# Performance work log

Measured on AMD Instinct MI355X. Metric: run time of the kernel, lower is better.

The kernel has to match this reference:

```python
import jax, jax.numpy as jnp
import numpy as np

B, T, F, H = 64, 128, 1024, 1024
FORGET_BIAS = 1.0  # TF BasicLSTMCell default


def setup_inputs() -> dict:
    key = jax.random.key(0)
    k1, k2 = jax.random.split(key, 2)
    x = jax.random.normal(k1, (B, T, F), dtype=jnp.float32)
    # single fused kernel weight [(F+H), 4H], TF gate order: i, j, f, o
    W = jax.random.uniform(k2, (F + H, 4 * H), dtype=jnp.float32, minval=-0.1, maxval=0.1)
    b = jnp.zeros((4 * H,), dtype=jnp.float32)
    return {"x": x, "W": W, "b": b}


def reference(x, W, b):
    # BasicLSTMCell unrolled over time (return_last=False, return_seq_2d=False)
    batch, n_steps, n_feat = x.shape
    n_hidden = W.shape[0] - n_feat

    def step(carry, xt):
        c, h = carry
        z = jnp.concatenate([xt, h], axis=1) @ W + b  # [B, 4H]
        i, j, f, o = jnp.split(z, 4, axis=1)
        c_new = c * jax.nn.sigmoid(f + FORGET_BIAS) + jax.nn.sigmoid(i) * jnp.tanh(j)
        h_new = jnp.tanh(c_new) * jax.nn.sigmoid(o)
        return (c_new, h_new), h_new

    c0 = jnp.zeros((batch, n_hidden), x.dtype)
    h0 = jnp.zeros((batch, n_hidden), x.dtype)
    _, hs = jax.lax.scan(step, (c0, h0), jnp.swapaxes(x, 0, 1))  # [T, B, H]
    return jnp.swapaxes(hs, 0, 1)  # [B, T, H]
```

## Files before the change

### kernel.cpp

```cpp
#include <hip/hip_runtime.h>
#include <hip/hip_bf16.h>

typedef unsigned short u16;
typedef unsigned int u32;
typedef unsigned long long u64;
typedef __bf16 bf16x8 __attribute__((ext_vector_type(8)));
typedef float f32x4 __attribute__((ext_vector_type(4)));

#define NB 64
#define NT 128
#define NF 1024
#define NH 1024
#define NK 2048
#define NG 4096
#define NBH (NB * NH)

#define FSTR 16

#define W_LDS_BYTES 131072
#define ZSX_BYTES (2 * 2 * 64 * 17 * 4)
#define ZSH_BYTES (2 * 64 * 17 * 4)
#define SMEM_BYTES (W_LDS_BYTES + ZSX_BYTES + ZSH_BYTES + 64)

__device__ __forceinline__ u16 f2bf(float f) {
  unsigned u = __builtin_bit_cast(unsigned, f);
  u = (u + 0x7FFFu + ((u >> 16) & 1u)) >> 16;
  return (u16)u;
}
__device__ __forceinline__ float bf2f(u16 v) {
  unsigned u = ((unsigned)v) << 16;
  return __builtin_bit_cast(float, u);
}

__global__ __launch_bounds__(256) void lstm_cvt_x(const float* __restrict__ x,
                                                  u16* __restrict__ xb) {
  int i = (blockIdx.x * 256 + threadIdx.x) * 4;
  float4 v = *reinterpret_cast<const float4*>(x + i);
  ushort4 o;
  o.x = f2bf(v.x); o.y = f2bf(v.y); o.z = f2bf(v.z); o.w = f2bf(v.w);
  *reinterpret_cast<ushort4*>(xb + i) = o;
}

__global__ __launch_bounds__(256) void lstm_prep_w(const float* __restrict__ W,
                                                   u16* __restrict__ wt_blk) {
  __shared__ float tile[32][33];
  int n0 = blockIdx.x * 32;
  int k0 = blockIdx.y * 32;
  int tc = threadIdx.x & 31;
  int tr = threadIdx.x >> 5;
#pragma unroll
  for (int i = 0; i < 4; ++i) {
    int k = tr + i * 8;
    tile[k][tc] = W[(size_t)(k0 + k) * NG + n0 + tc];
  }
  __syncthreads();
#pragma unroll
  for (int i = 0; i < 4; ++i) {
    int n = n0 + tr + i * 8;
    float wv = tile[tc][tr + i * 8];
    int k = k0 + tc;
    int g = n >> 10, col = n & 1023;
    int b = col >> 2, brow = g * 4 + (col & 3);
    int kh = k >> 10, ch = (k & 1023) >> 5;
    int slot = (k >> 3) & 3, elem = k & 7;
    size_t base = (size_t)b * 65536 + (size_t)(kh * 32 + ch) * 512
                + (size_t)(slot * 16 + brow) * 8 + elem;
    u16 hi = f2bf(wv);
    wt_blk[base] = hi;
    wt_blk[base + 32768] = f2bf(wv - bf2f(hi));
  }
}

__device__ __forceinline__ void mfma_pass(const u16* __restrict__ a0, size_t rstride,
                                          const u16* __restrict__ Wl, int khalf,
                                          int kq, int lane, f32x4 acc[4]) {
  bf16x8 pf[4], qf[4];
#pragma unroll
  for (int i = 0; i < 4; ++i)
    pf[i] = *reinterpret_cast<const bf16x8*>(a0 + (size_t)i * 16 * rstride);
#pragma unroll
  for (int cc = 0; cc < 8; ++cc) {
    if (cc < 7) {
#pragma unroll
      for (int i = 0; i < 4; ++i)
        qf[i] = *reinterpret_cast<const bf16x8*>(a0 + (size_t)i * 16 * rstride + (cc + 1) * 32);
    }
    const int ch = kq * 8 + cc;
    const bf16x8 wh = *reinterpret_cast<const bf16x8*>(
        Wl + (size_t)(khalf * 32 + ch) * 512 + lane * 8);
    const bf16x8 wl2 = *reinterpret_cast<const bf16x8*>(
        Wl + (size_t)(64 + khalf * 32 + ch) * 512 + lane * 8);
#pragma unroll
    for (int i = 0; i < 4; ++i)
      acc[i] = __builtin_amdgcn_mfma_f32_16x16x32_bf16(pf[i], wh, acc[i], 0, 0, 0);
#pragma unroll
    for (int i = 0; i < 4; ++i)
      acc[i] = __builtin_amdgcn_mfma_f32_16x16x32_bf16(pf[i], wl2, acc[i], 0, 0, 0);
#pragma unroll
    for (int i = 0; i < 4; ++i) pf[i] = qf[i];
  }
}

__global__ __launch_bounds__(512) void lstm_persist(
    const u16* __restrict__ xb, u16* __restrict__ hseq,
    const u16* __restrict__ wt_blk, const float* __restrict__ bias,
    float* __restrict__ out, u32* __restrict__ flags,
    float* __restrict__ zo) {
  extern __shared__ char smem[];
  u16* Wl = (u16*)smem;
  float (*zsx)[2][64][17] = (float(*)[2][64][17])(smem + W_LDS_BYTES);
  float (*zsh)[64][17] = (float(*)[64][17])(smem + W_LDS_BYTES + ZSX_BYTES);
  volatile u32* hsflag = (volatile u32*)(smem + W_LDS_BYTES + ZSX_BYTES + ZSH_BYTES);

  const int b = blockIdx.x;
  const int tid = threadIdx.x;
  const int lane = tid & 63;
  const int w = tid >> 6;
  const bool is_x = (w < 4);
  const int kq = w & 3;

  {
    const u16* src = wt_blk + (size_t)b * 65536;
#pragma unroll
    for (int it = 0; it < 16; ++it) {
      uint4 v = *reinterpret_cast<const uint4*>(src + (size_t)it * 4096 + tid * 8);
      *reinterpret_cast<uint4*>(Wl + (size_t)it * 4096 + tid * 8) = v;
    }
  }
  for (int i = tid; i < 2 * 64 * 17; i += 512) ((float*)zsh)[i] = 0.f;
  if (tid == 0) hsflag[0] = 0u;

  const int arow = lane & 15;
  const int kfr = 8 * (lane >> 4);
  const int kbase = kq * 256 + kfr;
  const int zn = lane & 15;
  const int mg = (lane >> 4) * 4;

  const int prow = tid >> 1;
  const int pc = (tid & 1) * 2;
  const int gc0 = b * 4 + pc;
  float bz[2][4];
  float creg[2] = {0.f, 0.f};
  if (tid < 128) {
#pragma unroll
    for (int j = 0; j < 2; ++j) {
      bz[j][0] = bias[gc0 + j];
      bz[j][1] = bias[NH + gc0 + j];
      bz[j][2] = bias[2 * NH + gc0 + j];
      bz[j][3] = bias[3 * NH + gc0 + j];
    }
  }
  __syncthreads();

  {
    f32x4 acc[4] = {};
    if (is_x) {
      const u16* a0 = xb + ((size_t)arow * NT + 0) * NF + kbase;
      mfma_pass(a0, (size_t)NT * NF, Wl, 0, kq, lane, acc);
      if (w < 2) {
#pragma unroll
        for (int i = 0; i < 4; ++i)
#pragma unroll
          for (int r = 0; r < 4; ++r) zsx[0][w][i * 16 + mg + r][zn] = acc[i][r];
      }
    }
    __syncthreads();
    if (is_x && w >= 2) {
#pragma unroll
      for (int i = 0; i < 4; ++i)
#pragma unroll
        for (int r = 0; r < 4; ++r) zsx[0][w - 2][i * 16 + mg + r][zn] += acc[i][r];
    }
    __syncthreads();
  }

#pragma unroll 1
  for (int t = 0; t < NT; ++t) {
    const int cb = t & 1;
    const int nb = (t + 1) & 1;
    f32x4 acc[4] = {};

    if (is_x) {
      if (t < NT - 1) {
        const u16* a0 = xb + ((size_t)arow * NT + (t + 1)) * NF + kbase;
        mfma_pass(a0, (size_t)NT * NF, Wl, 0, kq, lane, acc);
      }
    } else {
      if (t > 0) {
        const u32* fp = flags + ((size_t)t * 256 + kq * 64 + lane) * FSTR;
        u32 v = __hip_atomic_load(fp, __ATOMIC_RELAXED, __HIP_MEMORY_SCOPE_AGENT);
        while (!__all(v != 0)) {
          __builtin_amdgcn_s_sleep(1);
          v = __hip_atomic_load(fp, __ATOMIC_RELAXED, __HIP_MEMORY_SCOPE_AGENT);
        }

        const u64* hb = reinterpret_cast<const u64*>(hseq) + (size_t)t * (256 * 64);
        const int sbase = kq * 64 + 2 * (lane >> 4);
        u64 plo[4], phi[4], qlo[4], qhi[4];
#pragma unroll
        for (int i = 0; i < 4; ++i) {
          plo[i] = hb[(size_t)sbase * 64 + arow + 16 * i];
          phi[i] = hb[(size_t)(sbase + 1) * 64 + arow + 16 * i];
        }
        __builtin_amdgcn_s_setprio(1);
#pragma unroll
        for (int cc = 0; cc < 8; ++cc) {
          if (cc < 7) {
            const int s = sbase + (cc + 1) * 8;
#pragma unroll
            for (int i = 0; i < 4; ++i) {
              qlo[i] = hb[(size_t)s * 64 + arow + 16 * i];
              qhi[i] = hb[(size_t)(s + 1) * 64 + arow + 16 * i];
            }
          }
          const int ch = kq * 8 + cc;
          const bf16x8 wh = *reinterpret_cast<const bf16x8*>(
              Wl + (size_t)(32 + ch) * 512 + lane * 8);
          const bf16x8 wlo = *reinterpret_cast<const bf16x8*>(
              Wl + (size_t)(96 + ch) * 512 + lane * 8);
#pragma unroll
          for (int i = 0; i < 4; ++i) {
            union HU { u64 q[2]; bf16x8 f; } u;
            u.q[0] = plo[i];
            u.q[1] = phi[i];
            acc[i] = __builtin_amdgcn_mfma_f32_16x16x32_bf16(u.f, wh, acc[i], 0, 0, 0);
            acc[i] = __builtin_amdgcn_mfma_f32_16x16x32_bf16(u.f, wlo, acc[i], 0, 0, 0);
          }
#pragma unroll
          for (int i = 0; i < 4; ++i) { plo[i] = qlo[i]; phi[i] = qhi[i]; }
        }
        __builtin_amdgcn_s_setprio(0);
      }
    }

    if (is_x) {
      if (w < 2 && t < NT - 1) {
#pragma unroll
        for (int i = 0; i < 4; ++i)
#pragma unroll
          for (int r = 0; r < 4; ++r) zsx[nb][w][i * 16 + mg + r][zn] = acc[i][r];
      }
    } else {
      if (w < 6 && t > 0) {
#pragma unroll
        for (int i = 0; i < 4; ++i)
#pragma unroll
          for (int r = 0; r < 4; ++r) zsh[w - 4][i * 16 + mg + r][zn] = acc[i][r];
      }
    }
    __syncthreads();
    if (is_x) {
      if (w >= 2 && t < NT - 1) {
#pragma unroll
        for (int i = 0; i < 4; ++i)
#pragma unroll
          for (int r = 0; r < 4; ++r) zsx[nb][w - 2][i * 16 + mg + r][zn] += acc[i][r];
      }
    } else {
      if (w >= 6 && t > 0) {
#pragma unroll
        for (int i = 0; i < 4; ++i)
#pragma unroll
          for (int r = 0; r < 4; ++r) zsh[w - 6][i * 16 + mg + r][zn] += acc[i][r];
      }
    }
    __syncthreads();

    if (tid < 128) {
      float hn[2];
#pragma unroll
      for (int jj = 0; jj < 2; ++jj) {
        const int col = pc + jj;
        const float zi = zsx[cb][0][prow][col]      + zsx[cb][1][prow][col]      + zsh[0][prow][col]      + zsh[1][prow][col]      + bz[jj][0];
        const float zj = zsx[cb][0][prow][4 + col]  + zsx[cb][1][prow][4 + col]  + zsh[0][prow][4 + col]  + zsh[1][prow][4 + col]  + bz[jj][1];
        const float zf = zsx[cb][0][prow][8 + col]  + zsx[cb][1][prow][8 + col]  + zsh[0][prow][8 + col]  + zsh[1][prow][8 + col]  + bz[jj][2];
        const float zo4 = zsx[cb][0][prow][12 + col] + zsx[cb][1][prow][12 + col] + zsh[0][prow][12 + col] + zsh[1][prow][12 + col] + bz[jj][3];
        const float si = 1.f / (1.f + __expf(-zi));
        const float tj = tanhf(zj);
        const float sf = 1.f / (1.f + __expf(-(zf + 1.0f)));
        const float so = 1.f / (1.f + __expf(-zo4));
        const float cn = creg[jj] * sf + si * tj;
        hn[jj] = tanhf(cn) * so;
        creg[jj] = cn;
      }
      if (t < NT - 1) {
        u32 hv = (u32)f2bf(hn[0]) | ((u32)f2bf(hn[1]) << 16);
        u32* hp = reinterpret_cast<u32*>(hseq)
                + ((size_t)(t + 1) * 256 + b) * 128 + prow * 2 + (pc >> 1);
        __hip_atomic_store(hp, hv, __ATOMIC_RELAXED, __HIP_MEMORY_SCOPE_AGENT);
        asm volatile("s_waitcnt vmcnt(0)" ::: "memory");
        if (tid == 64) hsflag[0] = (u32)(t + 1);
        if (tid == 0) {
          while (hsflag[0] != (u32)(t + 1)) {}
          __hip_atomic_store(&flags[((size_t)(t + 1) * 256 + b) * FSTR], 1u,
                             __ATOMIC_RELAXED, __HIP_MEMORY_SCOPE_AGENT);
        }
      }
#pragma unroll
      for (int jj = 0; jj < 2; ++jj) {
        __hip_atomic_store(
            reinterpret_cast<u32*>(zo + ((size_t)t * NH + gc0 + jj) * NB + prow),
            __builtin_bit_cast(u32, hn[jj]),
            __ATOMIC_RELAXED, __HIP_MEMORY_SCOPE_AGENT);
      }
    }
  }

  __syncthreads();
  asm volatile("s_waitcnt vmcnt(0)" ::: "memory");
  if (tid == 0)
    __hip_atomic_store(&flags[(size_t)b * FSTR], 1u, __ATOMIC_RELAXED,
                       __HIP_MEMORY_SCOPE_AGENT);
  if (w == 0) {
    bool ok;
    do {
      u32 v0 = __hip_atomic_load(flags + (size_t)(lane * 4 + 0) * FSTR, __ATOMIC_RELAXED, __HIP_MEMORY_SCOPE_AGENT);
      u32 v1 = __hip_atomic_load(flags + (size_t)(lane * 4 + 1) * FSTR, __ATOMIC_RELAXED, __HIP_MEMORY_SCOPE_AGENT);
      u32 v2 = __hip_atomic_load(flags + (size_t)(lane * 4 + 2) * FSTR, __ATOMIC_RELAXED, __HIP_MEMORY_SCOPE_AGENT);
      u32 v3 = __hip_atomic_load(flags + (size_t)(lane * 4 + 3) * FSTR, __ATOMIC_RELAXED, __HIP_MEMORY_SCOPE_AGENT);
      ok = ((v0 & v1 & v2 & v3) == 1u);
      if (!__all(ok)) __builtin_amdgcn_s_sleep(1);
    } while (!__all(ok));
  }
  __syncthreads();

  {
    const int ts = b >> 1;
    const int r0 = (b & 1) * 32;
    float* T = (float*)smem;
#pragma unroll 4
    for (int it = 0; it < 16; ++it) {
      int flat = it * 512 + tid;
      int c = flat >> 3;
      int q = flat & 7;
      const u64* p = reinterpret_cast<const u64*>(
          zo + ((size_t)ts * NH + c) * NB + r0 + q * 4);
      u64 lo = __hip_atomic_load(p + 0, __ATOMIC_RELAXED, __HIP_MEMORY_SCOPE_AGENT);
      u64 hi = __hip_atomic_load(p + 1, __ATOMIC_RELAXED, __HIP_MEMORY_SCOPE_AGENT);
      T[(q * 4 + 0) * 1028 + c] = __builtin_bit_cast(float, (u32)lo);
      T[(q * 4 + 1) * 1028 + c] = __builtin_bit_cast(float, (u32)(lo >> 32));
      T[(q * 4 + 2) * 1028 + c] = __builtin_bit_cast(float, (u32)hi);
      T[(q * 4 + 3) * 1028 + c] = __builtin_bit_cast(float, (u32)(hi >> 32));
    }
    __syncthreads();
#pragma unroll 4
    for (int it = 0; it < 16; ++it) {
      int flat = it * 512 + tid;
      int r = flat >> 8;
      int c4 = flat & 255;
      float4 v;
      v.x = T[r * 1028 + c4 * 4 + 0];
      v.y = T[r * 1028 + c4 * 4 + 1];
      v.z = T[r * 1028 + c4 * 4 + 2];
      v.w = T[r * 1028 + c4 * 4 + 3];
      *reinterpret_cast<float4*>(
          out + ((size_t)(r0 + r) * NT + ts) * NH + c4 * 4) = v;
    }
  }
}

extern "C" void kernel_launch(void* const* d_in, const int* in_sizes, int n_in,
                              void* d_out, int out_size, void* d_ws, size_t ws_size,
                              hipStream_t stream) {
  const float* x = (const float*)d_in[0];
  const float* W = (const float*)d_in[1];
  const float* bias = (const float*)d_in[2];
  float* out = (float*)d_out;

  char* ws = (char*)d_ws;
  u16* xb = (u16*)(ws);
  u16* wt_blk = (u16*)(ws + 16777216);
  u16* hseq = (u16*)(ws + 50331648);
  u32* flags = (u32*)(ws + 67108864);
  float* zo = (float*)(ws + 69206016);

  hipMemsetAsync(hseq, 0, 256 * 512, stream);
  hipMemsetAsync(flags, 0, (size_t)NT * 256 * FSTR * 4, stream);

  lstm_cvt_x<<<(NB * NT * NF) / (256 * 4), 256, 0, stream>>>(x, xb);
  lstm_prep_w<<<dim3(NG / 32, NK / 32), 256, 0, stream>>>(W, wt_blk);

  hipFuncSetAttribute((const void*)lstm_persist,
                      hipFuncAttributeMaxDynamicSharedMemorySize, SMEM_BYTES);

  void* args[] = {(void*)&xb, (void*)&hseq, (void*)&wt_blk, (void*)&bias,
                  (void*)&out, (void*)&flags, (void*)&zo};
  hipLaunchCooperativeKernel((void*)lstm_persist, dim3(256), dim3(512), args,
                             SMEM_BYTES, stream);
}
```

Before: 1.038 ms.

## Reduce gate partials with LDS atomics and drop a per-step barrier

Replaces the two-stage store-then-add reduction of x and h gate partials into separate LDS buffers with float atomicAdd into a single double-buffered accumulator. One __syncthreads per timestep is removed. The x-waves now wait on per-wave release flags written by the pointwise waves after they zero the buffer slot, so the next step's x projection can overlap the pointwise phase. The cost is LDS atomic contention from eight waves adding into the same cells, and a reduction order that is no longer fixed.

```diff
diff --git a/kernel.cpp b/kernel.cpp
--- a/kernel.cpp
+++ b/kernel.cpp
@@ -18,9 +18,18 @@
 #define FSTR 16
 
 #define W_LDS_BYTES 131072
-#define ZSX_BYTES (2 * 2 * 64 * 17 * 4)
-#define ZSH_BYTES (2 * 64 * 17 * 4)
-#define SMEM_BYTES (W_LDS_BYTES + ZSX_BYTES + ZSH_BYTES + 64)
+#define ZS_BYTES (2 * 64 * 17 * 4)
+#define SMEM_BYTES (W_LDS_BYTES + ZS_BYTES + 64)
+
+__device__ __forceinline__ void st_rel(u32* p, u32 v) {
+  __hip_atomic_store(p, v, __ATOMIC_RELEASE, __HIP_MEMORY_SCOPE_WORKGROUP);
+}
+__device__ __forceinline__ u32 ld_acq(u32* p) {
+  return __hip_atomic_load(p, __ATOMIC_ACQUIRE, __HIP_MEMORY_SCOPE_WORKGROUP);
+}
+__device__ __forceinline__ void spin_ge(u32* p, u32 v) {
+  while (ld_acq(p) < v) {}
+}
 
 __device__ __forceinline__ u16 f2bf(float f) {
   unsigned u = __builtin_bit_cast(unsigned, f);
@@ -108,9 +117,8 @@
     float* __restrict__ zo) {
   extern __shared__ char smem[];
   u16* Wl = (u16*)smem;
-  float (*zsx)[2][64][17] = (float(*)[2][64][17])(smem + W_LDS_BYTES);
-  float (*zsh)[64][17] = (float(*)[64][17])(smem + W_LDS_BYTES + ZSX_BYTES);
-  volatile u32* hsflag = (volatile u32*)(smem + W_LDS_BYTES + ZSX_BYTES + ZSH_BYTES);
+  float (*zs)[64][17] = (float(*)[64][17])(smem + W_LDS_BYTES);
+  u32* st = (u32*)(smem + W_LDS_BYTES + ZS_BYTES);
 
   const int b = blockIdx.x;
   const int tid = threadIdx.x;
@@ -127,8 +135,8 @@
       *reinterpret_cast<uint4*>(Wl + (size_t)it * 4096 + tid * 8) = v;
     }
   }
-  for (int i = tid; i < 2 * 64 * 17; i += 512) ((float*)zsh)[i] = 0.f;
-  if (tid == 0) hsflag[0] = 0u;
+  for (int i = tid; i < 2 * 64 * 17; i += 512) ((float*)zs)[i] = 0.f;
+  if (tid < 16) st[tid] = 0u;
 
   const int arow = lane & 15;
   const int kfr = 8 * (lane >> 4);
@@ -152,38 +160,35 @@
   }
   __syncthreads();
 
-  {
+  if (is_x) {
     f32x4 acc[4] = {};
-    if (is_x) {
-      const u16* a0 = xb + ((size_t)arow * NT + 0) * NF + kbase;
-      mfma_pass(a0, (size_t)NT * NF, Wl, 0, kq, lane, acc);
-      if (w < 2) {
-#pragma unroll
-        for (int i = 0; i < 4; ++i)
-#pragma unroll
-          for (int r = 0; r < 4; ++r) zsx[0][w][i * 16 + mg + r][zn] = acc[i][r];
-      }
-    }
-    __syncthreads();
-    if (is_x && w >= 2) {
-#pragma unroll
-      for (int i = 0; i < 4; ++i)
-#pragma unroll
-        for (int r = 0; r < 4; ++r) zsx[0][w - 2][i * 16 + mg + r][zn] += acc[i][r];
-    }
-    __syncthreads();
-  }
+    const u16* a0 = xb + ((size_t)arow * NT + 0) * NF + kbase;
+    mfma_pass(a0, (size_t)NT * NF, Wl, 0, kq, lane, acc);
+#pragma unroll
+    for (int i = 0; i < 4; ++i)
+#pragma unroll
+      for (int r = 0; r < 4; ++r)
+        atomicAdd(&zs[0][i * 16 + mg + r][zn], acc[i][r]);
+  }
+  __syncthreads();
 
 #pragma unroll 1
   for (int t = 0; t < NT; ++t) {
     const int cb = t & 1;
     const int nb = (t + 1) & 1;
-    f32x4 acc[4] = {};
 
     if (is_x) {
       if (t < NT - 1) {
+        f32x4 acc[4] = {};
         const u16* a0 = xb + ((size_t)arow * NT + (t + 1)) * NF + kbase;
         mfma_pass(a0, (size_t)NT * NF, Wl, 0, kq, lane, acc);
+        spin_ge(&st[8], (u32)t);
+        spin_ge(&st[9], (u32)t);
+#pragma unroll
+        for (int i = 0; i < 4; ++i)
+#pragma unroll
+          for (int r = 0; r < 4; ++r)
+            atomicAdd(&zs[nb][i * 16 + mg + r][zn], acc[i][r]);
       }
     } else {
       if (t > 0) {
@@ -197,6 +202,7 @@
         const u64* hb = reinterpret_cast<const u64*>(hseq) + (size_t)t * (256 * 64);
         const int sbase = kq * 64 + 2 * (lane >> 4);
         u64 plo[4], phi[4], qlo[4], qhi[4];
+        f32x4 acc[4] = {};
 #pragma unroll
         for (int i = 0; i < 4; ++i) {
           plo[i] = hb[(size_t)sbase * 64 + arow + 16 * i];
@@ -230,40 +236,14 @@
           for (int i = 0; i < 4; ++i) { plo[i] = qlo[i]; phi[i] = qhi[i]; }
         }
         __builtin_amdgcn_s_setprio(0);
-      }
-    }
-
-    if (is_x) {
-      if (w < 2 && t < NT - 1) {
 #pragma unroll
         for (int i = 0; i < 4; ++i)
 #pragma unroll
-          for (int r = 0; r < 4; ++r) zsx[nb][w][i * 16 + mg + r][zn] = acc[i][r];
-      }
-    } else {
-      if (w < 6 && t > 0) {
-#pragma unroll
-        for (int i = 0; i < 4; ++i)
-#pragma unroll
-          for (int r = 0; r < 4; ++r) zsh[w - 4][i * 16 + mg + r][zn] = acc[i][r];
-      }
-    }
-    __syncthreads();
-    if (is_x) {
-      if (w >= 2 && t < NT - 1) {
-#pragma unroll
-        for (int i = 0; i < 4; ++i)
-#pragma unroll
-          for (int r = 0; r < 4; ++r) zsx[nb][w - 2][i * 16 + mg + r][zn] += acc[i][r];
-      }
-    } else {
-      if (w >= 6 && t > 0) {
-#pragma unroll
-        for (int i = 0; i < 4; ++i)
-#pragma unroll
-          for (int r = 0; r < 4; ++r) zsh[w - 6][i * 16 + mg + r][zn] += acc[i][r];
-      }
-    }
+          for (int r = 0; r < 4; ++r)
+            atomicAdd(&zs[cb][i * 16 + mg + r][zn], acc[i][r]);
+      }
+    }
+
     __syncthreads();
 
     if (tid < 128) {
@@ -271,10 +251,10 @@
 #pragma unroll
       for (int jj = 0; jj < 2; ++jj) {
         const int col = pc + jj;
-        const float zi = zsx[cb][0][prow][col]      + zsx[cb][1][prow][col]      + zsh[0][prow][col]      + zsh[1][prow][col]      + bz[jj][0];
-        const float zj = zsx[cb][0][prow][4 + col]  + zsx[cb][1][prow][4 + col]  + zsh[0][prow][4 + col]  + zsh[1][prow][4 + col]  + bz[jj][1];
-        const float zf = zsx[cb][0][prow][8 + col]  + zsx[cb][1][prow][8 + col]  + zsh[0][prow][8 + col]  + zsh[1][prow][8 + col]  + bz[jj][2];
-        const float zo4 = zsx[cb][0][prow][12 + col] + zsx[cb][1][prow][12 + col] + zsh[0][prow][12 + col] + zsh[1][prow][12 + col] + bz[jj][3];
+        const float zi = zs[cb][prow][col]      + bz[jj][0];
+        const float zj = zs[cb][prow][4 + col]  + bz[jj][1];
+        const float zf = zs[cb][prow][8 + col]  + bz[jj][2];
+        const float zo4 = zs[cb][prow][12 + col] + bz[jj][3];
         const float si = 1.f / (1.f + __expf(-zi));
         const float tj = tanhf(zj);
         const float sf = 1.f / (1.f + __expf(-(zf + 1.0f)));
@@ -289,13 +269,19 @@
                 + ((size_t)(t + 1) * 256 + b) * 128 + prow * 2 + (pc >> 1);
         __hip_atomic_store(hp, hv, __ATOMIC_RELAXED, __HIP_MEMORY_SCOPE_AGENT);
         asm volatile("s_waitcnt vmcnt(0)" ::: "memory");
-        if (tid == 64) hsflag[0] = (u32)(t + 1);
+        if (tid == 64) st_rel(&st[0], (u32)(t + 1));
         if (tid == 0) {
-          while (hsflag[0] != (u32)(t + 1)) {}
+          spin_ge(&st[0], (u32)(t + 1));
           __hip_atomic_store(&flags[((size_t)(t + 1) * 256 + b) * FSTR], 1u,
                              __ATOMIC_RELAXED, __HIP_MEMORY_SCOPE_AGENT);
         }
       }
+#pragma unroll
+      for (int g = 0; g < 4; ++g) {
+        zs[cb][prow][g * 4 + pc] = 0.f;
+        zs[cb][prow][g * 4 + pc + 1] = 0.f;
+      }
+      if (lane == 0) st_rel(&st[8 + w], (u32)(t + 1));
 #pragma unroll
       for (int jj = 0; jj < 2; ++jj) {
         __hip_atomic_store(
```

Result: slower. 1.913 ms (+84.2%).
